# Performance work log

Hardware: AMD Instinct MI355X
Metric: run time of the kernel (lower is better)

The kernel has to match this reference:

```python
import jax, jax.numpy as jnp
import numpy as np

H = 256      # hidden_size
L = 20       # max_length
V = 29       # output_size (vocab)
LAT = H + 8


def setup_inputs() -> dict:
    key = jax.random.key(0)
    ks = jax.random.split(key, 20)
    s = 0.05
    return {
        "input_tensor": jax.random.randint(ks[0], (1,), 0, V),
        "hidden": jax.random.normal(ks[1], (1, 1, H), dtype=jnp.float32),
        "encoder_outputs": jax.random.normal(ks[2], (L, H), dtype=jnp.float32),
        "cond": jax.random.randint(ks[3], (2,), 0, 4),
        "is_head": 1,
        # parameters (PyTorch Linear convention: weight [out, in])
        "emb": jax.random.normal(ks[4], (V, H), dtype=jnp.float32) * s,
        "w_l2d": jax.random.normal(ks[5], (H, LAT), dtype=jnp.float32) * s,
        "b_l2d": jnp.zeros((H,), dtype=jnp.float32),
        "w_attn": jax.random.normal(ks[6], (L, 2 * H), dtype=jnp.float32) * s,
        "b_attn": jnp.zeros((L,), dtype=jnp.float32),
        "w_comb": jax.random.normal(ks[7], (H, 2 * H), dtype=jnp.float32) * s,
        "b_comb": jnp.zeros((H,), dtype=jnp.float32),
        "w_ih": jax.random.normal(ks[8], (3 * H, H), dtype=jnp.float32) * s,
        "w_hh": jax.random.normal(ks[9], (3 * H, H), dtype=jnp.float32) * s,
        "b_ih": jnp.zeros((3 * H,), dtype=jnp.float32),
        "b_hh": jnp.zeros((3 * H,), dtype=jnp.float32),
        "w_out": jax.random.normal(ks[10], (V, H), dtype=jnp.float32) * s,
        "b_out": jnp.zeros((V,), dtype=jnp.float32),
    }


def gru_cell(x, h, w_ih, w_hh, b_ih, b_hh):
    # x, h: [1, H]; PyTorch GRU gate order: r, z, n
    gi = x @ w_ih.T + b_ih
    gh = h @ w_hh.T + b_hh
    ir, iz, inn = jnp.split(gi, 3, axis=-1)
    hr, hz, hn = jnp.split(gh, 3, axis=-1)
    r = jax.nn.sigmoid(ir + hr)
    z = jax.nn.sigmoid(iz + hz)
    n = jnp.tanh(inn + r * hn)
    return (1.0 - z) * n + z * h


def reference(input_tensor, hidden, encoder_outputs, cond, is_head,
              emb, w_l2d, b_l2d, w_attn, b_attn, w_comb, b_comb,
              w_ih, w_hh, b_ih, b_hh, w_out, b_out):
    if is_head:
        c = jnp.concatenate([jax.nn.one_hot(cond[0], 4),
                             jax.nn.one_hot(cond[1], 4)]).astype(hidden.dtype)  # [8]
        hidden = jnp.concatenate([hidden, c[None, None, :]], axis=2)  # [1,1,H+8]
        hidden = hidden @ w_l2d.T + b_l2d                              # [1,1,H]
    embedded = emb[input_tensor].reshape(1, 1, -1)                     # [1,1,H] (dropout: eval mode)
    attn_in = jnp.concatenate([embedded[0], hidden[0]], axis=1)        # [1,2H]
    attn_weights = jax.nn.softmax(attn_in @ w_attn.T + b_attn, axis=1) # [1,L]
    attn_applied = attn_weights @ encoder_outputs                      # [1,H]
    output = jnp.concatenate([embedded[0], attn_applied], axis=1)      # [1,2H]
    output = jax.nn.relu(output @ w_comb.T + b_comb)                   # [1,H]
    h_new = gru_cell(output, hidden[0], w_ih, w_hh, b_ih, b_hh)        # [1,H]
    logits = jax.nn.log_softmax(h_new @ w_out.T + b_out, axis=1)       # [1,V]
    return logits, h_new[None], attn_weights
```

## Files before the change

### kernel.cpp

```cpp
#include <hip/hip_runtime.h>
#include <hip/hip_bf16.h>

#define H 256
#define L 20
#define V 29
#define LAT 264
#define NBLK 97
#define NTHR 256
#define PZN 0xAAAAAAAAu


__device__ __forceinline__ float wave_sum(float v) {
#pragma unroll
    for (int o = 32; o > 0; o >>= 1) v += __shfl_down(v, o, 64);
    return v;
}

__device__ __forceinline__ void stws(float* p, float v) {
    __hip_atomic_store(p, v, __ATOMIC_RELAXED, __HIP_MEMORY_SCOPE_AGENT);
}

__device__ __forceinline__ float pollf(const float* p) {
    union { unsigned u; float f; } v;
    long spins = 0;
    for (;;) {
        v.u = __hip_atomic_load((const unsigned*)p, __ATOMIC_RELAXED,
                                __HIP_MEMORY_SCOPE_AGENT);
        if (v.u != PZN) break;
        __builtin_amdgcn_s_sleep(1);
        if (++spins > 5000000L) break;
    }
    return v.f;
}

__device__ __forceinline__ void copy_g2l4(float* dst, const float* src, int nfloats) {
    const float4* s4 = (const float4*)src;
    float4* d4 = (float4*)dst;
    const int n4 = nfloats >> 2;
    for (int i = threadIdx.x; i < n4; i += NTHR) d4[i] = s4[i];
}

__global__ __launch_bounds__(NTHR) void decoder_step(
    const int* inp, const float* hidden, const float* enc,
    const int* cond, const int* is_head,
    const float* emb, const float* w_l2d, const float* b_l2d,
    const float* w_attn, const float* b_attn,
    const float* w_comb, const float* b_comb,
    const float* w_ih, const float* w_hh,
    const float* b_ih, const float* b_hh,
    const float* w_out, const float* b_out,
    float* ws, float* out)
{
    extern __shared__ float sm[];
    const int b = blockIdx.x;
    const int t = threadIdx.x;
    const int wave = t >> 6, lane = t & 63;

    if (b < 32) {
        const int c0 = b * 8;
        if (is_head[0]) {
            float x0 = hidden[lane],       x1 = hidden[64 + lane];
            float x2 = hidden[128 + lane], x3 = hidden[192 + lane];
            float x4 = 0.f;
            if (lane < 8) {
                int c = (lane < 4) ? cond[0] : cond[1];
                x4 = (c == (lane & 3)) ? 1.f : 0.f;
            }
#pragma unroll
            for (int q = 0; q < 2; ++q) {
                int r = c0 + wave * 2 + q;
                const float* wr = w_l2d + r * LAT;
                float s = wr[lane] * x0 + wr[64 + lane] * x1
                        + wr[128 + lane] * x2 + wr[192 + lane] * x3;
                if (lane < 8) s += wr[256 + lane] * x4;
                s = wave_sum(s);
                if (lane == 0) stws(&ws[r], s + b_l2d[r]);
            }
        } else {
            if (t < 8) stws(&ws[c0 + t], hidden[c0 + t]);
        }

    } else if (b < 64) {
        const int k = b - 32, r0 = k * 8;
        float* wah  = sm;
        float* encl = sm + 5120;
        float* wcl  = sm + 10240;
        float* xatt = sm + 14336;
        float* bc   = sm + 14848;
        float* lge  = sm + 14864;
        float* lg   = sm + 14896;
        float* aw   = sm + 14928;
        for (int i = t; i < L * 64; i += NTHR) {
            int r = i >> 6, q = i & 63;
            ((float4*)wah)[r * 64 + q] = ((const float4*)(w_attn + r * 2 * H + H))[q];
        }
        copy_g2l4(encl, enc, L * H);
        copy_g2l4(wcl, w_comb + r0 * 2 * H, 8 * 2 * H);
        xatt[t] = emb[inp[0] * H + t];
        if (t < 8) bc[t] = b_comb[r0 + t];
        __syncthreads();
        for (int r = wave; r < L; r += 4) {
            float s = 0.f;
#pragma unroll
            for (int j = lane; j < H; j += 64) s += w_attn[r * 2 * H + j] * xatt[j];
            s = wave_sum(s);
            if (lane == 0) lge[r] = s + b_attn[r];
        }
        xatt[H + t] = pollf(ws + t);
        __syncthreads();
        for (int r = wave; r < L; r += 4) {
            float s = 0.f;
#pragma unroll
            for (int j = lane; j < H; j += 64) s += wah[r * H + j] * xatt[H + j];
            s = wave_sum(s);
            if (lane == 0) lg[r] = lge[r] + s;
        }
        __syncthreads();
        if (wave == 0) {
            float v = (lane < L) ? lg[lane] : -1e30f;
            float m = v;
#pragma unroll
            for (int o = 32; o > 0; o >>= 1) m = fmaxf(m, __shfl_xor(m, o, 64));
            float e = (lane < L) ? __expf(v - m) : 0.f;
            float ssum = e;
#pragma unroll
            for (int o = 32; o > 0; o >>= 1) ssum += __shfl_xor(ssum, o, 64);
            if (lane < L) {
                float a = e / ssum;
                aw[lane] = a;
                if (k == 0) out[V + H + lane] = a;
            }
        }
        __syncthreads();
        {
            float s = 0.f;
#pragma unroll
            for (int l = 0; l < L; ++l) s += aw[l] * encl[l * H + t];
            xatt[H + t] = s;
        }
        __syncthreads();
#pragma unroll
        for (int q = 0; q < 2; ++q) {
            int r = wave * 2 + q;
            float s = 0.f;
#pragma unroll
            for (int j = lane; j < 2 * H; j += 64) s += wcl[r * 2 * H + j] * xatt[j];
            s = wave_sum(s);
            if (lane == 0) stws(&ws[512 + r0 + r], fmaxf(s + bc[r], 0.f));
        }

    } else if (b < 96) {
        const int k = b - 64, c0 = k * 8;
        float* wh  = sm;
        float* wi  = sm + 6144;
        float* xh  = sm + 12288;
        float* xo  = sm + 12544;
        float* bbh = sm + 12800;
        float* bbi = sm + 12824;
        float* ghs = sm + 12848;
        float* gis = sm + 12872;
        copy_g2l4(wh,          w_hh + c0 * H,           8 * H);
        copy_g2l4(wh + 8 * H,  w_hh + (H + c0) * H,     8 * H);
        copy_g2l4(wh + 16 * H, w_hh + (2 * H + c0) * H, 8 * H);
        copy_g2l4(wi,          w_ih + c0 * H,           8 * H);
        copy_g2l4(wi + 8 * H,  w_ih + (H + c0) * H,     8 * H);
        copy_g2l4(wi + 16 * H, w_ih + (2 * H + c0) * H, 8 * H);
        if (t < 24) { int g = t >> 3, i = t & 7; bbh[t] = b_hh[g * H + c0 + i]; }
        if (t >= 32 && t < 56) {
            int u = t - 32, g = u >> 3, i = u & 7;
            bbi[u] = b_ih[g * H + c0 + i];
        }
        xh[t] = pollf(ws + t);
        __syncthreads();
#pragma unroll
        for (int q = 0; q < 6; ++q) {
            int m = wave * 6 + q;
            float s = 0.f;
#pragma unroll
            for (int j = lane; j < H; j += 64) s += wh[m * H + j] * xh[j];
            s = wave_sum(s);
            if (lane == 0) ghs[m] = s + bbh[m];
        }
        xo[t] = pollf(ws + 512 + t);
        __syncthreads();
#pragma unroll
        for (int q = 0; q < 6; ++q) {
            int m = wave * 6 + q;
            float s = 0.f;
#pragma unroll
            for (int j = lane; j < H; j += 64) s += wi[m * H + j] * xo[j];
            s = wave_sum(s);
            if (lane == 0) gis[m] = s + bbi[m];
        }
        __syncthreads();
        if (t < 8) {
            float r = 1.f / (1.f + __expf(-(gis[t] + ghs[t])));
            float z = 1.f / (1.f + __expf(-(gis[8 + t] + ghs[8 + t])));
            float n = tanhf(gis[16 + t] + r * ghs[16 + t]);
            float h = (1.f - z) * n + z * xh[c0 + t];
            out[V + c0 + t] = h;
            stws(&ws[768 + c0 + t], h);
        }

    } else {
        float* wo = sm;
        float* bo = sm + 7424;
        float* hn = sm + 7456;
        float* lg = sm + 7712;
        copy_g2l4(wo, w_out, V * H);
        if (t < V) bo[t] = b_out[t];
        hn[t] = pollf(ws + 768 + t);
        __syncthreads();
        for (int r = wave; r < V; r += 4) {
            float s = 0.f;
#pragma unroll
            for (int j = lane; j < H; j += 64) s += wo[r * H + j] * hn[j];
            s = wave_sum(s);
            if (lane == 0) lg[r] = s + bo[r];
        }
        __syncthreads();
        if (wave == 0) {
            float v = (lane < V) ? lg[lane] : -1e30f;
            float m = v;
#pragma unroll
            for (int o = 32; o > 0; o >>= 1) m = fmaxf(m, __shfl_xor(m, o, 64));
            float e = (lane < V) ? __expf(v - m) : 0.f;
            float s2 = e;
#pragma unroll
            for (int o = 32; o > 0; o >>= 1) s2 += __shfl_xor(s2, o, 64);
            float ls = logf(s2);
            if (lane < V) out[lane] = v - m - ls;
        }
    }
}

extern "C" void kernel_launch(void* const* d_in, const int* in_sizes, int n_in,
                              void* d_out, int out_size, void* d_ws, size_t ws_size,
                              hipStream_t stream) {
    const int* inp      = (const int*)d_in[0];
    const float* hidden = (const float*)d_in[1];
    const float* enc    = (const float*)d_in[2];
    const int* cond     = (const int*)d_in[3];
    const int* is_head  = (const int*)d_in[4];
    const float* emb    = (const float*)d_in[5];
    const float* w_l2d  = (const float*)d_in[6];
    const float* b_l2d  = (const float*)d_in[7];
    const float* w_attn = (const float*)d_in[8];
    const float* b_attn = (const float*)d_in[9];
    const float* w_comb = (const float*)d_in[10];
    const float* b_comb = (const float*)d_in[11];
    const float* w_ih   = (const float*)d_in[12];
    const float* w_hh   = (const float*)d_in[13];
    const float* b_ih   = (const float*)d_in[14];
    const float* b_hh   = (const float*)d_in[15];
    const float* w_out  = (const float*)d_in[16];
    const float* b_out  = (const float*)d_in[17];

    float* ws = (float*)d_ws;
    float* out = (float*)d_out;

    const size_t smem = 14960 * sizeof(float);
    decoder_step<<<NBLK, NTHR, smem, stream>>>(
        inp, hidden, enc, cond, is_head, emb, w_l2d, b_l2d, w_attn, b_attn,
        w_comb, b_comb, w_ih, w_hh, b_ih, b_hh, w_out, b_out, ws, out);
}
```

Measured before the change: 106.2 us.

## Stage weights with direct global-to-LDS loads and wave-local float4 dot products

New measurement: 104.0 us (median of 2 runs). -2.1%, faster.

```diff
diff --git a/kernel.cpp b/kernel.cpp
--- a/kernel.cpp
+++ b/kernel.cpp
@@ -1,5 +1,4 @@
 #include <hip/hip_runtime.h>
-#include <hip/hip_bf16.h>
 
 #define H 256
 #define L 20
@@ -10,10 +9,33 @@
 #define PZN 0xAAAAAAAAu
 
 
-__device__ __forceinline__ float wave_sum(float v) {
-#pragma unroll
-    for (int o = 32; o > 0; o >>= 1) v += __shfl_down(v, o, 64);
+typedef __attribute__((address_space(3))) unsigned int lds_u32;
+typedef __attribute__((address_space(1))) unsigned int glb_u32;
+
+__device__ __forceinline__ void g2l(const float* g, float* l, int lane) {
+    __builtin_amdgcn_global_load_lds(
+        (glb_u32*)(unsigned long long)(g + 4 * lane),
+        (lds_u32*)l, 16, 0, 0);
+}
+
+__device__ __forceinline__ float wsum(float v) {
+#pragma unroll
+    for (int o = 32; o > 0; o >>= 1) v += __shfl_xor(v, o, 64);
     return v;
+}
+
+__device__ __forceinline__ float wmax(float v) {
+#pragma unroll
+    for (int o = 32; o > 0; o >>= 1) v = fmaxf(v, __shfl_xor(v, o, 64));
+    return v;
+}
+
+__device__ __forceinline__ float dot44(float4 a, float4 b) {
+    return a.x * b.x + a.y * b.y + a.z * b.z + a.w * b.w;
+}
+
+__device__ __forceinline__ float dot4(float4 a, float b0, float b1, float b2, float b3) {
+    return a.x * b0 + a.y * b1 + a.z * b2 + a.w * b3;
 }
 
 __device__ __forceinline__ void stws(float* p, float v) {
@@ -31,13 +53,6 @@
         if (++spins > 5000000L) break;
     }
     return v.f;
-}
-
-__device__ __forceinline__ void copy_g2l4(float* dst, const float* src, int nfloats) {
-    const float4* s4 = (const float4*)src;
-    float4* d4 = (float4*)dst;
-    const int n4 = nfloats >> 2;
-    for (int i = threadIdx.x; i < n4; i += NTHR) d4[i] = s4[i];
 }
 
 __global__ __launch_bounds__(NTHR) void decoder_step(
@@ -59,21 +74,20 @@
     if (b < 32) {
         const int c0 = b * 8;
         if (is_head[0]) {
-            float x0 = hidden[lane],       x1 = hidden[64 + lane];
-            float x2 = hidden[128 + lane], x3 = hidden[192 + lane];
-            float x4 = 0.f;
+            const float4 x4 = ((const float4*)hidden)[lane];
+            float xt = 0.f;
             if (lane < 8) {
                 int c = (lane < 4) ? cond[0] : cond[1];
-                x4 = (c == (lane & 3)) ? 1.f : 0.f;
+                xt = (c == (lane & 3)) ? 1.f : 0.f;
             }
 #pragma unroll
             for (int q = 0; q < 2; ++q) {
                 int r = c0 + wave * 2 + q;
                 const float* wr = w_l2d + r * LAT;
-                float s = wr[lane] * x0 + wr[64 + lane] * x1
-                        + wr[128 + lane] * x2 + wr[192 + lane] * x3;
-                if (lane < 8) s += wr[256 + lane] * x4;
-                s = wave_sum(s);
+                float4 w4 = ((const float4*)wr)[lane];
+                float s = dot44(w4, x4);
+                if (lane < 8) s += wr[256 + lane] * xt;
+                s = wsum(s);
                 if (lane == 0) stws(&ws[r], s + b_l2d[r]);
             }
         } else {
@@ -82,117 +96,130 @@
 
     } else if (b < 64) {
         const int k = b - 32, r0 = k * 8;
-        float* wah  = sm;
-        float* encl = sm + 5120;
+        float* encl = sm;
+        float* wah  = sm + 5120;
         float* wcl  = sm + 10240;
-        float* xatt = sm + 14336;
-        float* bc   = sm + 14848;
-        float* lge  = sm + 14864;
-        float* lg   = sm + 14896;
-        float* aw   = sm + 14928;
-        for (int i = t; i < L * 64; i += NTHR) {
-            int r = i >> 6, q = i & 63;
-            ((float4*)wah)[r * 64 + q] = ((const float4*)(w_attn + r * 2 * H + H))[q];
-        }
-        copy_g2l4(encl, enc, L * H);
-        copy_g2l4(wcl, w_comb + r0 * 2 * H, 8 * 2 * H);
-        xatt[t] = emb[inp[0] * H + t];
-        if (t < 8) bc[t] = b_comb[r0 + t];
+        float* lg   = sm + 14336;
+
+#pragma unroll
+        for (int i = 0; i < 5; ++i) {
+            int r = wave * 5 + i;
+            g2l(enc + r * H, encl + r * H, lane);
+            g2l(w_attn + r * 2 * H + H, wah + r * H, lane);
+        }
+#pragma unroll
+        for (int q = 0; q < 2; ++q) {
+            int cr = wave * 2 + q;
+            const float* src = w_comb + (r0 + cr) * 2 * H;
+            g2l(src,     wcl + cr * 2 * H,     lane);
+            g2l(src + H, wcl + cr * 2 * H + H, lane);
+        }
+
+        const float* erow = emb + inp[0] * H;
+        const float4 e4 = ((const float4*)erow)[lane];
+        float bcq[2];
+#pragma unroll
+        for (int q = 0; q < 2; ++q) bcq[q] = b_comb[r0 + wave * 2 + q];
+        float lge[5];
+#pragma unroll
+        for (int i = 0; i < 5; ++i) {
+            int r = wave * 5 + i;
+            float4 w4 = ((const float4*)(w_attn + r * 2 * H))[lane];
+            lge[i] = wsum(dot44(w4, e4)) + b_attn[r];
+        }
+
+        float h0 = pollf(ws + 4 * lane);
+        float h1 = pollf(ws + 4 * lane + 1);
+        float h2 = pollf(ws + 4 * lane + 2);
+        float h3 = pollf(ws + 4 * lane + 3);
+        asm volatile("s_waitcnt vmcnt(0)" ::: "memory");
+
+#pragma unroll
+        for (int i = 0; i < 5; ++i) {
+            int r = wave * 5 + i;
+            float4 w4 = ((const float4*)(wah + r * H))[lane];
+            float s = wsum(dot4(w4, h0, h1, h2, h3));
+            if (lane == 0) lg[r] = lge[i] + s;
+        }
         __syncthreads();
-        for (int r = wave; r < L; r += 4) {
-            float s = 0.f;
-#pragma unroll
-            for (int j = lane; j < H; j += 64) s += w_attn[r * 2 * H + j] * xatt[j];
-            s = wave_sum(s);
-            if (lane == 0) lge[r] = s + b_attn[r];
-        }
-        xatt[H + t] = pollf(ws + t);
-        __syncthreads();
-        for (int r = wave; r < L; r += 4) {
-            float s = 0.f;
-#pragma unroll
-            for (int j = lane; j < H; j += 64) s += wah[r * H + j] * xatt[H + j];
-            s = wave_sum(s);
-            if (lane == 0) lg[r] = lge[r] + s;
-        }
-        __syncthreads();
-        if (wave == 0) {
-            float v = (lane < L) ? lg[lane] : -1e30f;
-            float m = v;
-#pragma unroll
-            for (int o = 32; o > 0; o >>= 1) m = fmaxf(m, __shfl_xor(m, o, 64));
-            float e = (lane < L) ? __expf(v - m) : 0.f;
-            float ssum = e;
-#pragma unroll
-            for (int o = 32; o > 0; o >>= 1) ssum += __shfl_xor(ssum, o, 64);
-            if (lane < L) {
-                float a = e / ssum;
-                aw[lane] = a;
-                if (k == 0) out[V + H + lane] = a;
-            }
-        }
-        __syncthreads();
-        {
-            float s = 0.f;
-#pragma unroll
-            for (int l = 0; l < L; ++l) s += aw[l] * encl[l * H + t];
-            xatt[H + t] = s;
-        }
-        __syncthreads();
+
+        float v = (lane < L) ? lg[lane] : -1e30f;
+        float m = wmax(v);
+        float e = (lane < L) ? __expf(v - m) : 0.f;
+        float inv = 1.f / wsum(e);
+        if (k == 0 && wave == 0 && lane < L) out[V + H + lane] = e * inv;
+
+        float4 app = make_float4(0.f, 0.f, 0.f, 0.f);
+#pragma unroll
+        for (int l = 0; l < L; ++l) {
+            float a = __shfl(e, l, 64) * inv;
+            float4 ev = ((const float4*)(encl + l * H))[lane];
+            app.x += a * ev.x; app.y += a * ev.y;
+            app.z += a * ev.z; app.w += a * ev.w;
+        }
+
 #pragma unroll
         for (int q = 0; q < 2; ++q) {
-            int r = wave * 2 + q;
-            float s = 0.f;
-#pragma unroll
-            for (int j = lane; j < 2 * H; j += 64) s += wcl[r * 2 * H + j] * xatt[j];
-            s = wave_sum(s);
-            if (lane == 0) stws(&ws[512 + r0 + r], fmaxf(s + bc[r], 0.f));
+            int cr = wave * 2 + q;
+            float4 wa = ((const float4*)(wcl + cr * 2 * H))[lane];
+            float4 wb = ((const float4*)(wcl + cr * 2 * H + H))[lane];
+            float s = wsum(dot44(wa, e4) + dot44(wb, app));
+            if (lane == 0) stws(&ws[512 + r0 + cr], fmaxf(s + bcq[q], 0.f));
         }
 
     } else if (b < 96) {
         const int k = b - 64, c0 = k * 8;
         float* wh  = sm;
         float* wi  = sm + 6144;
-        float* xh  = sm + 12288;
-        float* xo  = sm + 12544;
-        float* bbh = sm + 12800;
-        float* bbi = sm + 12824;
-        float* ghs = sm + 12848;
-        float* gis = sm + 12872;
-        copy_g2l4(wh,          w_hh + c0 * H,           8 * H);
-        copy_g2l4(wh + 8 * H,  w_hh + (H + c0) * H,     8 * H);
-        copy_g2l4(wh + 16 * H, w_hh + (2 * H + c0) * H, 8 * H);
-        copy_g2l4(wi,          w_ih + c0 * H,           8 * H);
-        copy_g2l4(wi + 8 * H,  w_ih + (H + c0) * H,     8 * H);
-        copy_g2l4(wi + 16 * H, w_ih + (2 * H + c0) * H, 8 * H);
-        if (t < 24) { int g = t >> 3, i = t & 7; bbh[t] = b_hh[g * H + c0 + i]; }
-        if (t >= 32 && t < 56) {
-            int u = t - 32, g = u >> 3, i = u & 7;
-            bbi[u] = b_ih[g * H + c0 + i];
-        }
-        xh[t] = pollf(ws + t);
+        float* ghs = sm + 12288;
+        float* gis = sm + 12320;
+        float* xh  = sm + 12352;
+
+#pragma unroll
+        for (int i = 0; i < 6; ++i) {
+            int mm = wave * 6 + i;
+            int g = mm >> 3, rr = c0 + (mm & 7);
+            g2l(w_hh + (g * H + rr) * H, wh + mm * H, lane);
+            g2l(w_ih + (g * H + rr) * H, wi + mm * H, lane);
+        }
+        float bh[6], bi[6];
+#pragma unroll
+        for (int i = 0; i < 6; ++i) {
+            int mm = wave * 6 + i;
+            int g = mm >> 3;
+            bh[i] = b_hh[g * H + c0 + (mm & 7)];
+            bi[i] = b_ih[g * H + c0 + (mm & 7)];
+        }
+
+        float h0 = pollf(ws + 4 * lane);
+        float h1 = pollf(ws + 4 * lane + 1);
+        float h2 = pollf(ws + 4 * lane + 2);
+        float h3 = pollf(ws + 4 * lane + 3);
+        if (wave == 0) ((float4*)xh)[lane] = make_float4(h0, h1, h2, h3);
+        asm volatile("s_waitcnt vmcnt(0)" ::: "memory");
+
+#pragma unroll
+        for (int i = 0; i < 6; ++i) {
+            int mm = wave * 6 + i;
+            float4 w4 = ((const float4*)(wh + mm * H))[lane];
+            float s = wsum(dot4(w4, h0, h1, h2, h3));
+            if (lane == 0) ghs[mm] = s + bh[i];
+        }
+
+        float o0 = pollf(ws + 512 + 4 * lane);
+        float o1 = pollf(ws + 512 + 4 * lane + 1);
+        float o2 = pollf(ws + 512 + 4 * lane + 2);
+        float o3 = pollf(ws + 512 + 4 * lane + 3);
+
+#pragma unroll
+        for (int i = 0; i < 6; ++i) {
+            int mm = wave * 6 + i;
+            float4 w4 = ((const float4*)(wi + mm * H))[lane];
+            float s = wsum(dot4(w4, o0, o1, o2, o3));
+            if (lane == 0) gis[mm] = s + bi[i];
+        }
         __syncthreads();
-#pragma unroll
-        for (int q = 0; q < 6; ++q) {
-            int m = wave * 6 + q;
-            float s = 0.f;
-#pragma unroll
-            for (int j = lane; j < H; j += 64) s += wh[m * H + j] * xh[j];
-            s = wave_sum(s);
-            if (lane == 0) ghs[m] = s + bbh[m];
-        }
-        xo[t] = pollf(ws + 512 + t);
-        __syncthreads();
-#pragma unroll
-        for (int q = 0; q < 6; ++q) {
-            int m = wave * 6 + q;
-            float s = 0.f;
-#pragma unroll
-            for (int j = lane; j < H; j += 64) s += wi[m * H + j] * xo[j];
-            s = wave_sum(s);
-            if (lane == 0) gis[m] = s + bbi[m];
-        }
-        __syncthreads();
+
         if (t < 8) {
             float r = 1.f / (1.f + __expf(-(gis[t] + ghs[t])));
             float z = 1.f / (1.f + __expf(-(gis[8 + t] + ghs[8 + t])));
@@ -204,30 +231,28 @@
 
     } else {
         float* wo = sm;
-        float* bo = sm + 7424;
-        float* hn = sm + 7456;
-        float* lg = sm + 7712;
-        copy_g2l4(wo, w_out, V * H);
-        if (t < V) bo[t] = b_out[t];
-        hn[t] = pollf(ws + 768 + t);
-        __syncthreads();
+        float* lg = sm + 7424;
+        for (int r = wave; r < V; r += 4)
+            g2l(w_out + r * H, wo + r * H, lane);
+        float bo = (lane < V) ? b_out[lane] : 0.f;
+
+        float n0 = pollf(ws + 768 + 4 * lane);
+        float n1 = pollf(ws + 768 + 4 * lane + 1);
+        float n2 = pollf(ws + 768 + 4 * lane + 2);
+        float n3 = pollf(ws + 768 + 4 * lane + 3);
+        asm volatile("s_waitcnt vmcnt(0)" ::: "memory");
+
         for (int r = wave; r < V; r += 4) {
-            float s = 0.f;
-#pragma unroll
-            for (int j = lane; j < H; j += 64) s += wo[r * H + j] * hn[j];
-            s = wave_sum(s);
-            if (lane == 0) lg[r] = s + bo[r];
+            float4 w4 = ((const float4*)(wo + r * H))[lane];
+            float s = wsum(dot4(w4, n0, n1, n2, n3));
+            if (lane == 0) lg[r] = s;
         }
         __syncthreads();
         if (wave == 0) {
-            float v = (lane < V) ? lg[lane] : -1e30f;
-            float m = v;
-#pragma unroll
-            for (int o = 32; o > 0; o >>= 1) m = fmaxf(m, __shfl_xor(m, o, 64));
+            float v = (lane < V) ? lg[lane] + bo : -1e30f;
+            float m = wmax(v);
             float e = (lane < V) ? __expf(v - m) : 0.f;
-            float s2 = e;
-#pragma unroll
-            for (int o = 32; o > 0; o >>= 1) s2 += __shfl_xor(s2, o, 64);
+            float s2 = wsum(e);
             float ls = logf(s2);
             if (lane < V) out[lane] = v - m - ls;
         }
@@ -259,7 +284,7 @@
     float* ws = (float*)d_ws;
     float* out = (float*)d_out;
 
-    const size_t smem = 14960 * sizeof(float);
+    const size_t smem = 14368 * sizeof(float);
     decoder_step<<<NBLK, NTHR, smem, stream>>>(
         inp, hidden, enc, cond, is_head, emb, w_l2d, b_l2d, w_attn, b_attn,
         w_comb, b_comb, w_ih, w_hh, b_ih, b_hh, w_out, b_out, ws, out);
```
